# Performance work log

Hardware: AMD Instinct MI355X
Metric: run time of the kernel (lower is better)

The kernel has to match this reference:

```python
import jax, jax.numpy as jnp
import numpy as np

CODEBOOK_SIZE = 4096
CODE_DIM = 256
N = 65536
COMMITMENT_COST = 0.25


def setup_inputs() -> dict:
    key = jax.random.key(0)
    k1, k2 = jax.random.split(key)
    z_flat = jax.random.normal(k1, (N, CODE_DIM), dtype=jnp.float32)
    # embedding initialized uniform(-1/codebook_size, 1/codebook_size) as in torch module
    emb_weight = jax.random.uniform(
        k2, (CODEBOOK_SIZE, CODE_DIM), dtype=jnp.float32,
        minval=-1.0 / CODEBOOK_SIZE, maxval=1.0 / CODEBOOK_SIZE)
    return {"z_flat": z_flat, "emb_weight": emb_weight}


def reference(z_flat, emb_weight):
    # squared L2 distances: [N, K] = |z|^2 + |e|^2 - 2 z e^T
    distances = (
        jnp.sum(z_flat ** 2, axis=1, keepdims=True)
        + jnp.sum(emb_weight ** 2, axis=1)
        - 2.0 * jnp.matmul(z_flat, emb_weight.T)
    )
    indices = jnp.argmin(distances, axis=1)  # [N]
    quantized = emb_weight[indices]          # [N, code_dim]

    e_latent_loss = jnp.mean((jax.lax.stop_gradient(quantized) - z_flat) ** 2)
    q_latent_loss = jnp.mean((quantized - jax.lax.stop_gradient(z_flat)) ** 2)
    loss = q_latent_loss + COMMITMENT_COST * e_latent_loss

    # straight-through estimator
    quantized_st = z_flat + jax.lax.stop_gradient(quantized - z_flat)
    return (loss, quantized_st, indices)
```

## Files before the change

### kernel.cpp

```cpp
#include <hip/hip_runtime.h>

#define KCODES 4096
#define DIM    256
#define NROWS  65536
#define MARGIN 4.0e-4f
#define DSLACK 3.0e-5f
#define LCAP   4096
#define CPAD   32
#define LSTRIDE (DIM + 4)

typedef unsigned long long u64;
typedef unsigned int  uint;
typedef unsigned short ushort;
typedef __attribute__((ext_vector_type(8))) short bf16x8;
typedef __attribute__((ext_vector_type(4))) float f32x4;

typedef __attribute__((address_space(3))) uint lds_u32_t;
typedef __attribute__((address_space(1))) uint glb_u32_t;

__device__ __forceinline__ void g2lds16(const void* g, void* l) {
    __builtin_amdgcn_global_load_lds((const glb_u32_t*)g, (lds_u32_t*)l, 16, 0, 0);
}

__device__ __forceinline__ float dppmin_quad(float m) {
    m = fminf(m, __int_as_float(__builtin_amdgcn_update_dpp(0, __float_as_int(m), 0xB1, 0xF, 0xF, true)));
    m = fminf(m, __int_as_float(__builtin_amdgcn_update_dpp(0, __float_as_int(m), 0x4E, 0xF, 0xF, true)));
    return m;
}
__device__ __forceinline__ float dppmin_row16(float m) {
    m = fminf(m, __int_as_float(__builtin_amdgcn_update_dpp(0, __float_as_int(m), 0x124, 0xF, 0xF, true)));
    m = fminf(m, __int_as_float(__builtin_amdgcn_update_dpp(0, __float_as_int(m), 0x128, 0xF, 0xF, true)));
    return m;
}
__device__ __forceinline__ uint dppor_row16(uint v) {
    v |= (uint)__builtin_amdgcn_update_dpp(0, (int)v, 0x124, 0xF, 0xF, true);
    v |= (uint)__builtin_amdgcn_update_dpp(0, (int)v, 0x128, 0xF, 0xF, true);
    return v;
}


__device__ __forceinline__ float np_half_sum128(const float4* __restrict__ p4) {
    #pragma clang fp contract(off)
    float4 v0 = p4[0], v1 = p4[1];
    float r0 = v0.x * v0.x, r1 = v0.y * v0.y, r2 = v0.z * v0.z, r3 = v0.w * v0.w;
    float r4 = v1.x * v1.x, r5 = v1.y * v1.y, r6 = v1.z * v1.z, r7 = v1.w * v1.w;
    #pragma unroll
    for (int i = 1; i < 16; ++i) {
        float4 a = p4[2 * i], b = p4[2 * i + 1];
        r0 += a.x * a.x; r1 += a.y * a.y; r2 += a.z * a.z; r3 += a.w * a.w;
        r4 += b.x * b.x; r5 += b.y * b.y; r6 += b.z * b.z; r7 += b.w * b.w;
    }
    return ((r0 + r1) + (r2 + r3)) + ((r4 + r5) + (r6 + r7));
}

__global__ void k_rownorm(const float* __restrict__ src, float* __restrict__ dst, int nrows) {
    int r = blockIdx.x * blockDim.x + threadIdx.x;
    if (r >= nrows) return;
    const float4* p4 = (const float4*)(src + (size_t)r * DIM);
    float s;
    {
        #pragma clang fp contract(off)
        s = np_half_sum128(p4) + np_half_sum128(p4 + 32);
    }
    dst[r] = s;
}

__device__ __forceinline__ float f32_dist(float Cr, float ebc, double accv) {
    #pragma clang fp contract(off)
    float A = Cr + ebc;
    float B = 2.0f * (float)accv;
    return A - B;
}

__device__ __forceinline__ ushort f2bf(float f) {
    uint u = __float_as_uint(f);
    return (ushort)((u + 0x7fffu + ((u >> 16) & 1u)) >> 16);
}


__global__ void k_split(const float* __restrict__ src, ushort* __restrict__ dst, int n8) {
    int i = blockIdx.x * blockDim.x + threadIdx.x;
    if (i >= n8) return;
    const float4* s4 = (const float4*)src;
    float4 a = s4[2 * i], b = s4[2 * i + 1];
    uint4 ov;
    ov.x = (uint)f2bf(a.x) | ((uint)f2bf(a.y) << 16);
    ov.y = (uint)f2bf(a.z) | ((uint)f2bf(a.w) << 16);
    ov.z = (uint)f2bf(b.x) | ((uint)f2bf(b.y) << 16);
    ov.w = (uint)f2bf(b.z) | ((uint)f2bf(b.w) << 16);
    *(uint4*)&dst[8 * i] = ov;
}

__global__ void k_init(int* __restrict__ cnt) {
    cnt[blockIdx.x * 256 + threadIdx.x] = 0;
}

__global__ __launch_bounds__(256, 2)
void k_gemm(const ushort* __restrict__ zh, const ushort* __restrict__ eh,
            const float* __restrict__ Crow, const float* __restrict__ eb2,
            float* __restrict__ tk, uint* __restrict__ tk2) {
    __shared__ __align__(16) ushort Bs[2][64 * 256];

    const int t = threadIdx.x;
    const int lane = t & 63;
    const int w = t >> 6;
    const int l15 = lane & 15, l4 = lane >> 4;
    const int row0w = blockIdx.x * 128 + w * 32;

    const char* ebp = (const char*)eh;

    auto stage = [&](int buf, int ct2) {
        const char* base = ebp + (size_t)ct2 * 64 * 512;
        #pragma unroll
        for (int i = 0; i < 8; ++i) {
            int idx = i * 256 + t;
            int code = idx >> 5;
            int c16  = idx & 31;
            int src  = (code << 9) + ((c16 ^ (code & 7)) << 4);
            g2lds16(base + src, (char*)Bs[buf] + idx * 16);
        }
    };

    bf16x8 a[2][8];
    #pragma unroll
    for (int f = 0; f < 2; ++f)
        #pragma unroll
        for (int ks = 0; ks < 8; ++ks)
            a[f][ks] = *(const bf16x8*)&zh[(size_t)(row0w + f * 16 + l15) * 256 + ks * 32 + l4 * 8];

    float crf[8];
    #pragma unroll
    for (int f = 0; f < 2; ++f)
        #pragma unroll
        for (int rg = 0; rg < 4; ++rg)
            crf[f * 4 + rg] = Crow[row0w + f * 16 + l4 * 4 + rg];

    float mprev[8];
    const f32x4 fzero = (f32x4){0.f, 0.f, 0.f, 0.f};
    f32x4 accA[2][4], accB[2][4];
    float ebvA[4], ebvB[4];

    auto ksloop = [&](const ushort* Bb, f32x4 (&acc)[2][4]) {
        #pragma unroll
        for (int ks = 0; ks < 8; ++ks) {
            bf16x8 bfv[4];
            #pragma unroll
            for (int cg = 0; cg < 4; ++cg) {
                int rB = cg * 16 + l15;
                int off = rB * 256 + ((ks * 32 + l4 * 8) ^ ((l15 & 7) << 3));
                bfv[cg] = *(const bf16x8*)&Bb[off];
            }
            __builtin_amdgcn_s_setprio(1);
            #pragma unroll
            for (int f = 0; f < 2; ++f)
                #pragma unroll
                for (int cg = 0; cg < 4; ++cg)
                    acc[f][cg] = __builtin_amdgcn_mfma_f32_16x16x32_bf16(
                        a[f][ks], bfv[cg], ks == 0 ? fzero : acc[f][cg], 0, 0, 0);
            __builtin_amdgcn_s_setprio(0);
        }
    };

    auto epi = [&](f32x4 (&acc)[2][4], const float (&ebv)[4], int ct2, bool odd) {
        #pragma unroll
        for (int f = 0; f < 2; ++f) {
            #pragma unroll
            for (int rg = 0; rg < 4; ++rg) {
                float m =    fmaf(-2.0f, acc[f][0][rg], ebv[0]);
                m = fminf(m, fmaf(-2.0f, acc[f][1][rg], ebv[1]));
                m = fminf(m, fmaf(-2.0f, acc[f][2][rg], ebv[2]));
                m = fminf(m, fmaf(-2.0f, acc[f][3][rg], ebv[3]));
                m = dppmin_quad(m);
                if (!odd) {
                    mprev[f * 4 + rg] = m;
                } else {
                    m = fminf(m, mprev[f * 4 + rg]);
                    float mt = dppmin_row16(m);
                    int q = (int)((m - mt) * 1e5f);
                    q = q > 255 ? 255 : q;
                    uint pk = (uint)q << (8 * (l15 >> 2));
                    pk = dppor_row16(pk);
                    if (l15 == 0) {
                        int grow = row0w + f * 16 + l4 * 4 + rg;
                        int tt = ct2 >> 1;
                        tk [(size_t)tt * NROWS + grow] = crf[f * 4 + rg] + mt;
                        tk2[(size_t)tt * NROWS + grow] = pk;
                    }
                }
            }
        }
    };

    stage(0, 0);
    #pragma unroll
    for (int cg = 0; cg < 4; ++cg) ebvA[cg] = eb2[cg * 16 + l15];
    __syncthreads();

    for (int tp = 0; tp < 32; ++tp) {
        int t0 = 2 * tp;
        stage(1, t0 + 1);
        if (tp > 0) epi(accB, ebvB, t0 - 1, true);
        ksloop(Bs[0], accA);
        __syncthreads();

        if (tp < 31) stage(0, t0 + 2);
        #pragma unroll
        for (int cg = 0; cg < 4; ++cg) ebvB[cg] = eb2[(t0 + 1) * 64 + cg * 16 + l15];
        epi(accA, ebvA, t0, false);
        if (tp < 31) {
            #pragma unroll
            for (int cg = 0; cg < 4; ++cg) ebvA[cg] = eb2[(t0 + 2) * 64 + cg * 16 + l15];
        }
        ksloop(Bs[1], accB);
        __syncthreads();
    }
    epi(accB, ebvB, 63, true);
}

__global__ void k_lists(const float* __restrict__ tk, const uint* __restrict__ tk2,
                        int* __restrict__ cnt, int* __restrict__ list,
                        u64* __restrict__ fkey) {
    int row = blockIdx.x * 256 + threadIdx.x;
    int lane = threadIdx.x & 63;
    float tm[32]; uint pk[32];
    #pragma unroll
    for (int tt = 0; tt < 32; ++tt) {
        tm[tt] = tk [(size_t)tt * NROWS + row];
        pk[tt] = tk2[(size_t)tt * NROWS + row];
    }
    float best = tm[0];
    #pragma unroll
    for (int tt = 1; tt < 32; ++tt) best = fminf(best, tm[tt]);
    fkey[row] = ~0ull;
    float cutoff = best + (MARGIN + DSLACK);

    #pragma unroll
    for (int tt = 0; tt < 32; ++tt) {
        #pragma unroll
        for (int p = 0; p < 4; ++p) {
            float v = tm[tt] + (float)((pk[tt] >> (8 * p)) & 255u) * 1e-5f;
            bool pred = v <= cutoff;
            u64 mask = __ballot(pred);
            if (mask) {
                int sub = tt * 4 + p;
                int nq = __popcll(mask);
                int rank = __popcll(mask & ((1ull << lane) - 1ull));
                int base = 0;
                if (lane == 0) base = atomicAdd(&cnt[sub * CPAD], nq);
                base = __shfl(base, 0, 64);
                int pos = base + rank;
                if (pred && pos < LCAP) list[sub * LCAP + pos] = row;
            }
        }
    }
}

__global__ __launch_bounds__(256, 2)
void k_exact(const float* __restrict__ z, const float* __restrict__ e,
             const float* __restrict__ Crow, const float* __restrict__ eb2,
             const int* __restrict__ list, const int* __restrict__ cnt,
             u64* __restrict__ fkey) {
    __shared__ __align__(16) float ex[32][260];
    __shared__ __align__(16) float zx[32][260];
    __shared__ int rows[32];
    __shared__ u64 keytab[32][17];
    const int sub = blockIdx.x;
    const int tile = sub >> 2, qq = sub & 3;
    const int nct = cnt[sub * CPAD];
    const int t = threadIdx.x;
    const int rp = t & 15, cs = t >> 4;

    {
        int cc = t >> 3, c8 = t & 7;
        int gcode = tile * 128 + (cc >> 2) * 16 + qq * 4 + (cc & 3);
        const float4* src = (const float4*)(e + (size_t)gcode * DIM);
        float4* dr = (float4*)ex[cc];
        #pragma unroll
        for (int j = 0; j < 8; ++j) dr[c8 + 8 * j] = src[c8 + 8 * j];
    }
    const int gc0 = tile * 128 + (cs >> 2) * 16 + qq * 4 + (cs & 3);
    const int gc1 = tile * 128 + ((cs >> 2) + 4) * 16 + qq * 4 + (cs & 3);
    const float ebc0 = eb2[gc0];
    const float ebc1 = eb2[gc1];

    for (int base = blockIdx.y * 32; base < nct; base += gridDim.y * 32) {
        __syncthreads();
        if (t < 32) {
            int i = base + t;
            rows[t] = list[sub * LCAP + (i < nct ? i : nct - 1)];
        }
        __syncthreads();
        {
            int rr = t >> 3, c8 = t & 7;
            const float4* src = (const float4*)(z + (size_t)rows[rr] * DIM);
            float4* dr = (float4*)zx[rr];
            #pragma unroll
            for (int j = 0; j < 8; ++j) dr[c8 + 8 * j] = src[c8 + 8 * j];
        }
        __syncthreads();

        double a00 = 0.0, a01 = 0.0, a10 = 0.0, a11 = 0.0;
        const float4* z0 = (const float4*)zx[rp];
        const float4* z1 = (const float4*)zx[rp + 16];
        const float4* e0 = (const float4*)ex[cs];
        const float4* e1 = (const float4*)ex[cs + 16];
        #pragma unroll 8
        for (int d4 = 0; d4 < 64; ++d4) {
            float4 x0 = z0[d4], x1 = z1[d4], y0 = e0[d4], y1 = e1[d4];
            a00 += (double)x0.x * (double)y0.x; a00 += (double)x0.y * (double)y0.y;
            a00 += (double)x0.z * (double)y0.z; a00 += (double)x0.w * (double)y0.w;
            a01 += (double)x0.x * (double)y1.x; a01 += (double)x0.y * (double)y1.y;
            a01 += (double)x0.z * (double)y1.z; a01 += (double)x0.w * (double)y1.w;
            a10 += (double)x1.x * (double)y0.x; a10 += (double)x1.y * (double)y0.y;
            a10 += (double)x1.z * (double)y0.z; a10 += (double)x1.w * (double)y0.w;
            a11 += (double)x1.x * (double)y1.x; a11 += (double)x1.y * (double)y1.y;
            a11 += (double)x1.z * (double)y1.z; a11 += (double)x1.w * (double)y1.w;
        }
        int r0 = rows[rp], r1 = rows[rp + 16];
        float C0 = Crow[r0], C1 = Crow[r1];
        u64 k00 = ((u64)__float_as_uint(f32_dist(C0, ebc0, a00)) << 32) | (u64)gc0;
        u64 k01 = ((u64)__float_as_uint(f32_dist(C0, ebc1, a01)) << 32) | (u64)gc1;
        u64 k10 = ((u64)__float_as_uint(f32_dist(C1, ebc0, a10)) << 32) | (u64)gc0;
        u64 k11 = ((u64)__float_as_uint(f32_dist(C1, ebc1, a11)) << 32) | (u64)gc1;
        keytab[rp][cs]      = k00 < k01 ? k00 : k01;
        keytab[rp + 16][cs] = k10 < k11 ? k10 : k11;
        __syncthreads();
        if (t < 32) {
            u64 kb = keytab[t][0];
            #pragma unroll
            for (int j = 1; j < 16; ++j) {
                u64 k = keytab[t][j];
                kb = k < kb ? k : kb;
            }
            atomicMin((unsigned long long*)&fkey[rows[t]], kb);
        }
    }
}

__global__ __launch_bounds__(256)
void k_gather(const float* __restrict__ z, const float* __restrict__ e,
              const u64* __restrict__ fkey, float* __restrict__ out,
              double* __restrict__ partial) {
    __shared__ double lred[4];
    const int t = threadIdx.x;
    const int row = blockIdx.x * 32 + (t >> 3);
    const int c8 = t & 7;
    const int idx = (int)(fkey[row] & 0xffffffffull);
    if (c8 == 0) out[1 + (size_t)NROWS * DIM + row] = (float)idx;
    const float4* zr = (const float4*)(z + (size_t)row * DIM);
    const float4* er = (const float4*)(e + (size_t)idx * DIM);
    float4* orow = (float4*)(out + 1 + (size_t)row * DIM);
    double lacc = 0.0;
    #pragma unroll
    for (int j = 0; j < 8; ++j) {
        float4 q = er[c8 + 8 * j];
        float4 zv = zr[c8 + 8 * j];
        orow[c8 + 8 * j] = q;
        double d0 = (double)q.x - (double)zv.x;
        double d1 = (double)q.y - (double)zv.y;
        double d2 = (double)q.z - (double)zv.z;
        double d3 = (double)q.w - (double)zv.w;
        lacc += d0 * d0 + d1 * d1 + d2 * d2 + d3 * d3;
    }
    for (int off = 32; off > 0; off >>= 1) lacc += __shfl_down(lacc, off, 64);
    if ((t & 63) == 0) lred[t >> 6] = lacc;
    __syncthreads();
    if (t == 0) partial[blockIdx.x] = lred[0] + lred[1] + lred[2] + lred[3];
}

__global__ void k_finish(const double* __restrict__ partial, float* __restrict__ out, int n) {
    __shared__ double s[256];
    double a = 0.0;
    for (int i = threadIdx.x; i < n; i += 256) a += partial[i];
    s[threadIdx.x] = a;
    __syncthreads();
    for (int off = 128; off > 0; off >>= 1) {
        if (threadIdx.x < off) s[threadIdx.x] += s[threadIdx.x + off];
        __syncthreads();
    }
    if (threadIdx.x == 0)
        out[0] = (float)(1.25 * s[0] / ((double)NROWS * (double)DIM));
}


__global__ __launch_bounds__(256, 1)
void k_main_slow(const float* __restrict__ z, const float* __restrict__ e,
                 const float* __restrict__ Crow, const float* __restrict__ eb2,
                 float* __restrict__ out, double* __restrict__ partial) {
    __shared__ float  zt[64][LSTRIDE];
    __shared__ float  et[64][LSTRIDE];
    __shared__ float  redd[64][17];
    __shared__ int    redi[64][17];
    __shared__ int    bsel[64];
    __shared__ double lred[4];

    const int t  = threadIdx.x;
    const int tx = t & 15;
    const int ty = t >> 4;
    const int row0 = blockIdx.x * 64;

    {
        const float4* zsrc = (const float4*)(z + (size_t)row0 * DIM);
        for (int i = t; i < 64 * (DIM / 4); i += 256) {
            int r = i >> 6, c4 = i & 63;
            *(float4*)&zt[r][c4 * 4] = zsrc[r * (DIM / 4) + c4];
        }
    }
    float Cr[4];
    #pragma unroll
    for (int ri = 0; ri < 4; ++ri) Cr[ri] = Crow[row0 + ty * 4 + ri];
    float bestd[4]; int besti[4];
    #pragma unroll
    for (int ri = 0; ri < 4; ++ri) { bestd[ri] = __int_as_float(0x7f800000); besti[ri] = 0; }

    for (int kt = 0; kt < KCODES / 64; ++kt) {
        __syncthreads();
        {
            const float4* esrc = (const float4*)(e + (size_t)kt * 64 * DIM);
            for (int i = t; i < 64 * (DIM / 4); i += 256) {
                int r = i >> 6, c4 = i & 63;
                *(float4*)&et[r][c4 * 4] = esrc[r * (DIM / 4) + c4];
            }
        }
        __syncthreads();
        double acc[4][4];
        #pragma unroll
        for (int a = 0; a < 4; ++a)
            #pragma unroll
            for (int b = 0; b < 4; ++b) acc[a][b] = 0.0;
        #pragma unroll 4
        for (int d4 = 0; d4 < DIM / 4; ++d4) {
            float4 za[4], ea[4];
            #pragma unroll
            for (int ri = 0; ri < 4; ++ri) za[ri] = *(const float4*)&zt[ty * 4 + ri][d4 * 4];
            #pragma unroll
            for (int ci = 0; ci < 4; ++ci) ea[ci] = *(const float4*)&et[tx + 16 * ci][d4 * 4];
            #pragma unroll
            for (int ri = 0; ri < 4; ++ri)
                #pragma unroll
                for (int ci = 0; ci < 4; ++ci)
                    acc[ri][ci] += (double)za[ri].x * (double)ea[ci].x
                                 + (double)za[ri].y * (double)ea[ci].y
                                 + (double)za[ri].z * (double)ea[ci].z
                                 + (double)za[ri].w * (double)ea[ci].w;
        }
        #pragma unroll
        for (int ci = 0; ci < 4; ++ci) {
            int c = kt * 64 + tx + 16 * ci;
            float ebc = eb2[c];
            #pragma unroll
            for (int ri = 0; ri < 4; ++ri) {
                float d = f32_dist(Cr[ri], ebc, acc[ri][ci]);
                if (d < bestd[ri]) { bestd[ri] = d; besti[ri] = c; }
            }
        }
    }
    __syncthreads();
    #pragma unroll
    for (int ri = 0; ri < 4; ++ri) {
        redd[ty * 4 + ri][tx] = bestd[ri];
        redi[ty * 4 + ri][tx] = besti[ri];
    }
    __syncthreads();
    if (t < 64) {
        float bd = redd[t][0]; int bi = redi[t][0];
        for (int j = 1; j < 16; ++j) {
            float d = redd[t][j]; int i2 = redi[t][j];
            if (d < bd || (d == bd && i2 < bi)) { bd = d; bi = i2; }
        }
        bsel[t] = bi;
        out[1 + (size_t)NROWS * DIM + row0 + t] = (float)bi;
    }
    __syncthreads();
    double lacc = 0.0;
    {
        int r = t >> 2, qd = (t & 3) * 64;
        int bi = bsel[r];
        const float* qrow = e + (size_t)bi * DIM + qd;
        float* orow = out + 1 + (size_t)(row0 + r) * DIM + qd;
        #pragma unroll 4
        for (int d = 0; d < 64; ++d) {
            float qv = qrow[d], zv = zt[r][qd + d];
            double df = (double)qv - (double)zv;
            lacc += df * df;
            orow[d] = qv;
        }
    }
    for (int off = 32; off > 0; off >>= 1) lacc += __shfl_down(lacc, off, 64);
    if ((t & 63) == 0) lred[t >> 6] = lacc;
    __syncthreads();
    if (t == 0) partial[blockIdx.x] = lred[0] + lred[1] + lred[2] + lred[3];
}


extern "C" void kernel_launch(void* const* d_in, const int* in_sizes, int n_in,
                              void* d_out, int out_size, void* d_ws, size_t ws_size,
                              hipStream_t stream) {
    const float* z = (const float*)d_in[0];
    const float* e = (const float*)d_in[1];
    float* out = (float*)d_out;
    char* w = (char*)d_ws;

    size_t o = 0;
    auto take = [&](size_t b) { size_t r = o; o = (o + b + 255) & ~(size_t)255; return r; };
    size_t o_zh = take((size_t)NROWS * DIM * 2);
    size_t o_eh = take((size_t)KCODES * DIM * 2);
    size_t o_cr = take((size_t)NROWS * 4);
    size_t o_eb = take((size_t)KCODES * 4);
    size_t o_tk = take((size_t)32 * NROWS * 4);
    size_t o_t2 = take((size_t)32 * NROWS * 4);
    size_t o_fk = take((size_t)NROWS * 8);
    size_t o_cn = take((size_t)128 * CPAD * 4);
    size_t o_ls = take((size_t)128 * LCAP * 4);
    size_t o_pt = take((size_t)2048 * 8);
    size_t need = o;

    if (ws_size >= need) {
        ushort* zh = (ushort*)(w + o_zh);
        ushort* eh = (ushort*)(w + o_eh);
        float* Cr  = (float*)(w + o_cr);
        float* eb  = (float*)(w + o_eb);
        float* tk  = (float*)(w + o_tk);
        uint*  tk2 = (uint*)(w + o_t2);
        u64*   fk  = (u64*)(w + o_fk);
        int*   cn  = (int*)(w + o_cn);
        int*   ls  = (int*)(w + o_ls);
        double* pt = (double*)(w + o_pt);

        k_split<<<NROWS * DIM / 8 / 256, 256, 0, stream>>>(z, zh, NROWS * DIM / 8);
        k_split<<<KCODES * DIM / 8 / 256, 256, 0, stream>>>(e, eh, KCODES * DIM / 8);
        k_rownorm<<<NROWS / 256, 256, 0, stream>>>(z, Cr, NROWS);
        k_rownorm<<<KCODES / 256, 256, 0, stream>>>(e, eb, KCODES);
        k_init<<<(128 * CPAD) / 256, 256, 0, stream>>>(cn);
        k_gemm<<<NROWS / 128, 256, 0, stream>>>(zh, eh, Cr, eb, tk, tk2);
        k_lists<<<NROWS / 256, 256, 0, stream>>>(tk, tk2, cn, ls, fk);
        dim3 ge(128, 16);
        k_exact<<<ge, 256, 0, stream>>>(z, e, Cr, eb, ls, cn, fk);
        k_gather<<<NROWS / 32, 256, 0, stream>>>(z, e, fk, out, pt);
        k_finish<<<1, 256, 0, stream>>>(pt, out, 2048);
    } else {
        float* Cr  = (float*)w;
        float* eb  = Cr + NROWS;
        double* pt = (double*)(eb + KCODES);
        k_rownorm<<<NROWS / 256, 256, 0, stream>>>(z, Cr, NROWS);
        k_rownorm<<<KCODES / 256, 256, 0, stream>>>(e, eb, KCODES);
        k_main_slow<<<NROWS / 64, 256, 0, stream>>>(z, e, Cr, eb, out, pt);
        k_finish<<<1, 256, 0, stream>>>(pt, out, NROWS / 64);
    }
}
```

Measured before the change: 330.0 us.

## Fuse bf16 conversion with row norms and merge candidate listing into GEMM

A new k_prep kernel replaces the separate bf16 split and row-norm kernels. Each thread handles one row, writing the bf16 copy and computing the squared norm in one pass, so z and e are read from global memory once instead of twice. The candidate-list building from k_lists now runs at the end of k_gemm, where 128 threads per block read back that block's top-k results, which removes a launch. The trade-offs: the per-row layout in k_prep gives less coalesced loads than the old flat split, the GEMM kernel carries a low-occupancy serial tail, and the norm summation order must still match what the exact-distance stage expects.

Result: no change. 331.4 us (+0.4%).

```diff
diff --git a/kernel.cpp b/kernel.cpp
--- a/kernel.cpp
+++ b/kernel.cpp
@@ -77,18 +77,44 @@
     return (ushort)((u + 0x7fffu + ((u >> 16) & 1u)) >> 16);
 }
 
-
-__global__ void k_split(const float* __restrict__ src, ushort* __restrict__ dst, int n8) {
-    int i = blockIdx.x * blockDim.x + threadIdx.x;
-    if (i >= n8) return;
-    const float4* s4 = (const float4*)src;
-    float4 a = s4[2 * i], b = s4[2 * i + 1];
+__device__ __forceinline__ uint4 pack8(float4 a, float4 b) {
     uint4 ov;
     ov.x = (uint)f2bf(a.x) | ((uint)f2bf(a.y) << 16);
     ov.y = (uint)f2bf(a.z) | ((uint)f2bf(a.w) << 16);
     ov.z = (uint)f2bf(b.x) | ((uint)f2bf(b.y) << 16);
     ov.w = (uint)f2bf(b.z) | ((uint)f2bf(b.w) << 16);
-    *(uint4*)&dst[8 * i] = ov;
+    return ov;
+}
+
+
+__global__ void k_prep(const float* __restrict__ src, ushort* __restrict__ dst,
+                       float* __restrict__ nrm, int nrows) {
+    int r = blockIdx.x * blockDim.x + threadIdx.x;
+    if (r >= nrows) return;
+    const float4* p4 = (const float4*)(src + (size_t)r * DIM);
+    uint4* d4 = (uint4*)(dst + (size_t)r * DIM);
+    float h[2];
+    #pragma unroll
+    for (int half = 0; half < 2; ++half) {
+        #pragma clang fp contract(off)
+        const float4* p = p4 + half * 32;
+        float4 v0 = p[0], v1 = p[1];
+        d4[half * 16] = pack8(v0, v1);
+        float r0 = v0.x * v0.x, r1 = v0.y * v0.y, r2 = v0.z * v0.z, r3 = v0.w * v0.w;
+        float r4 = v1.x * v1.x, r5 = v1.y * v1.y, r6 = v1.z * v1.z, r7 = v1.w * v1.w;
+        #pragma unroll
+        for (int i = 1; i < 16; ++i) {
+            float4 a = p[2 * i], b = p[2 * i + 1];
+            d4[half * 16 + i] = pack8(a, b);
+            r0 += a.x * a.x; r1 += a.y * a.y; r2 += a.z * a.z; r3 += a.w * a.w;
+            r4 += b.x * b.x; r5 += b.y * b.y; r6 += b.z * b.z; r7 += b.w * b.w;
+        }
+        h[half] = ((r0 + r1) + (r2 + r3)) + ((r4 + r5) + (r6 + r7));
+    }
+    {
+        #pragma clang fp contract(off)
+        nrm[r] = h[0] + h[1];
+    }
 }
 
 __global__ void k_init(int* __restrict__ cnt) {
@@ -98,7 +124,9 @@
 __global__ __launch_bounds__(256, 2)
 void k_gemm(const ushort* __restrict__ zh, const ushort* __restrict__ eh,
             const float* __restrict__ Crow, const float* __restrict__ eb2,
-            float* __restrict__ tk, uint* __restrict__ tk2) {
+            float* __restrict__ tk, uint* __restrict__ tk2,
+            int* __restrict__ cnt, int* __restrict__ list,
+            u64* __restrict__ fkey) {
     __shared__ __align__(16) ushort Bs[2][64 * 256];
 
     const int t = threadIdx.x;
@@ -215,41 +243,38 @@
         __syncthreads();
     }
     epi(accB, ebvB, 63, true);
-}
-
-__global__ void k_lists(const float* __restrict__ tk, const uint* __restrict__ tk2,
-                        int* __restrict__ cnt, int* __restrict__ list,
-                        u64* __restrict__ fkey) {
-    int row = blockIdx.x * 256 + threadIdx.x;
-    int lane = threadIdx.x & 63;
-    float tm[32]; uint pk[32];
-    #pragma unroll
-    for (int tt = 0; tt < 32; ++tt) {
-        tm[tt] = tk [(size_t)tt * NROWS + row];
-        pk[tt] = tk2[(size_t)tt * NROWS + row];
-    }
-    float best = tm[0];
-    #pragma unroll
-    for (int tt = 1; tt < 32; ++tt) best = fminf(best, tm[tt]);
-    fkey[row] = ~0ull;
-    float cutoff = best + (MARGIN + DSLACK);
-
-    #pragma unroll
-    for (int tt = 0; tt < 32; ++tt) {
-        #pragma unroll
-        for (int p = 0; p < 4; ++p) {
-            float v = tm[tt] + (float)((pk[tt] >> (8 * p)) & 255u) * 1e-5f;
-            bool pred = v <= cutoff;
-            u64 mask = __ballot(pred);
-            if (mask) {
-                int sub = tt * 4 + p;
-                int nq = __popcll(mask);
-                int rank = __popcll(mask & ((1ull << lane) - 1ull));
-                int base = 0;
-                if (lane == 0) base = atomicAdd(&cnt[sub * CPAD], nq);
-                base = __shfl(base, 0, 64);
-                int pos = base + rank;
-                if (pred && pos < LCAP) list[sub * LCAP + pos] = row;
+
+    __syncthreads();
+    if (t < 128) {
+        int row = blockIdx.x * 128 + t;
+        float tm[32]; uint pkv[32];
+        #pragma unroll
+        for (int tt = 0; tt < 32; ++tt) {
+            tm[tt]  = tk [(size_t)tt * NROWS + row];
+            pkv[tt] = tk2[(size_t)tt * NROWS + row];
+        }
+        float best = tm[0];
+        #pragma unroll
+        for (int tt = 1; tt < 32; ++tt) best = fminf(best, tm[tt]);
+        fkey[row] = ~0ull;
+        float cutoff = best + (MARGIN + DSLACK);
+        #pragma unroll
+        for (int tt = 0; tt < 32; ++tt) {
+            #pragma unroll
+            for (int p = 0; p < 4; ++p) {
+                float v = tm[tt] + (float)((pkv[tt] >> (8 * p)) & 255u) * 1e-5f;
+                bool pred = v <= cutoff;
+                u64 mask = __ballot(pred);
+                if (mask) {
+                    int sub = tt * 4 + p;
+                    int nq = __popcll(mask);
+                    int rank = __popcll(mask & ((1ull << lane) - 1ull));
+                    int base = 0;
+                    if (lane == 0) base = atomicAdd(&cnt[sub * CPAD], nq);
+                    base = __shfl(base, 0, 64);
+                    int pos = base + rank;
+                    if (pred && pos < LCAP) list[sub * LCAP + pos] = row;
+                }
             }
         }
     }
@@ -527,13 +552,10 @@
         int*   ls  = (int*)(w + o_ls);
         double* pt = (double*)(w + o_pt);
 
-        k_split<<<NROWS * DIM / 8 / 256, 256, 0, stream>>>(z, zh, NROWS * DIM / 8);
-        k_split<<<KCODES * DIM / 8 / 256, 256, 0, stream>>>(e, eh, KCODES * DIM / 8);
-        k_rownorm<<<NROWS / 256, 256, 0, stream>>>(z, Cr, NROWS);
-        k_rownorm<<<KCODES / 256, 256, 0, stream>>>(e, eb, KCODES);
+        k_prep<<<NROWS / 256, 256, 0, stream>>>(z, zh, Cr, NROWS);
+        k_prep<<<KCODES / 256, 256, 0, stream>>>(e, eh, eb, KCODES);
         k_init<<<(128 * CPAD) / 256, 256, 0, stream>>>(cn);
-        k_gemm<<<NROWS / 128, 256, 0, stream>>>(zh, eh, Cr, eb, tk, tk2);
-        k_lists<<<NROWS / 256, 256, 0, stream>>>(tk, tk2, cn, ls, fk);
+        k_gemm<<<NROWS / 128, 256, 0, stream>>>(zh, eh, Cr, eb, tk, tk2, cn, ls, fk);
         dim3 ge(128, 16);
         k_exact<<<ge, 256, 0, stream>>>(z, e, Cr, eb, ls, cn, fk);
         k_gather<<<NROWS / 32, 256, 0, stream>>>(z, e, fk, out, pt);
```
